# Optimization experiments

Hardware: AMD Instinct MI355X
Metric: run time of the kernel (lower is better)

The kernel has to match this reference:

```python
import jax, jax.numpy as jnp
import numpy as np

H = 768  # hidden size
L = 2    # num layers


def _lstm_layer(xs, ms, Wih, Whh, bih, bhh):
    """xs: [S,B,in], ms: [S,B,H] mask. Returns (outputs [S,B,H], (hT, cT)).
    PyTorch LSTMCell gate order: i, f, g, o. Zero initial state (module default),
    so the reset term init_hidden*(1-mask) is identically zero."""
    B = xs.shape[1]
    h0 = jnp.zeros((B, H), xs.dtype)
    c0 = jnp.zeros((B, H), xs.dtype)
    # Precompute input projections for all timesteps in one big GEMM.
    x_proj = jnp.einsum('sbi,gi->sbg', xs, Wih) + bih + bhh  # [S,B,4H]

    def step(carry, inp):
        h, c = carry
        xp, mt = inp
        gates = xp + h @ Whh.T  # [B,4H]
        i, f, g, o = jnp.split(gates, 4, axis=-1)
        i = jax.nn.sigmoid(i)
        f = jax.nn.sigmoid(f)
        g = jnp.tanh(g)
        o = jax.nn.sigmoid(o)
        c_next = (f * c + i * g)
        h_next = o * jnp.tanh(c_next)
        # mask-based state reset (h0=c0=0 -> pure multiply)
        h_next = h_next * mt
        c_next = c_next * mt
        return (h_next, c_next), h_next

    (hT, cT), outs = jax.lax.scan(step, (h0, c0), (x_proj, ms))
    return outs, (hT, cT)


def setup_inputs() -> dict:
    key = jax.random.key(0)
    ks = jax.random.split(key, 5)
    s = 0.05
    return {
        'x': jax.random.normal(ks[0], (64, 512, 768), jnp.float32),
        'mask': jnp.ones((64, 512), jnp.float32),
        'W_ih': jax.random.normal(ks[1], (L, 4 * H, 768), jnp.float32) * s,
        'W_hh': jax.random.normal(ks[2], (L, 4 * H, H), jnp.float32) * s,
        'b_ih': jax.random.normal(ks[3], (L, 4 * H), jnp.float32) * s,
        'b_hh': jax.random.normal(ks[4], (L, 4 * H), jnp.float32) * s,
    }


def reference(x, mask, W_ih, W_hh, b_ih, b_hh):
    # batch_first=True: transpose to [S,B,...]
    xs = jnp.transpose(x, (1, 0, 2))          # [S,B,in]
    ms = jnp.transpose(mask, (1, 0))[:, :, None]  # [S,B,1]
    ms = jnp.broadcast_to(ms, ms.shape[:2] + (H,))  # [S,B,H]
    hn, cn = [], []
    inp = xs
    for l in range(L):
        outs, (hT, cT) = _lstm_layer(inp, ms, W_ih[l], W_hh[l], b_ih[l], b_hh[l])
        hn.append(hT)
        cn.append(cT)
        inp = outs
    output = jnp.transpose(inp, (1, 0, 2))  # [B,S,H]
    return output, (jnp.stack(hn, 0), jnp.stack(cn, 0))
```

## Files before the change

### kernel.cpp

```cpp
#include <hip/hip_runtime.h>
#include <hip/hip_bf16.h>


#define HID 768
#define FH  3072
#define SEQ 512
#define BAT 64
#define GB  16
#define WPG 64
#define CPW 12
#define NWG 256
#define TPB 768
#define WBLK (12*64*8)

typedef __attribute__((ext_vector_type(8))) __bf16 bf16x8;
typedef __attribute__((ext_vector_type(4))) float f32x4;
typedef unsigned int u32;
typedef unsigned long long u64;

__device__ __forceinline__ float sigm(float z) { return 1.f / (1.f + __expf(-z)); }
__device__ __forceinline__ float tanh_fast(float x) {
  float a = fabsf(x);
  float e = __expf(-2.f * a);
  float t = (1.f - e) / (1.f + e);
  return copysignf(t, x);
}
__device__ __forceinline__ unsigned short bfbits(__bf16 b) {
  union { __bf16 b; unsigned short s; } u; u.b = b; return u.s;
}
__device__ __forceinline__ __bf16 bits2bf(unsigned short s) {
  union { unsigned short s; __bf16 b; } u; u.s = s; return u.b;
}
__device__ __forceinline__ u32 packsplit(float v) {
  __bf16 h = (__bf16)v;
  __bf16 l = (__bf16)(v - (float)h);
  return ((u32)bfbits(h) << 16) | (u32)bfbits(l);
}
__device__ __forceinline__ void split8(const float* p, bf16x8& hi, bf16x8& lo) {
  const float4* q = (const float4*)p;
  float4 a = q[0], b = q[1];
  float v[8] = {a.x, a.y, a.z, a.w, b.x, b.y, b.z, b.w};
#pragma unroll
  for (int i = 0; i < 8; ++i) {
    __bf16 h = (__bf16)v[i];
    hi[i] = h;
    lo[i] = (__bf16)(v[i] - (float)h);
  }
}
__device__ __forceinline__ void unpack8(const u32 w[8], bf16x8& hi, bf16x8& lo) {
#pragma unroll
  for (int i = 0; i < 8; ++i) {
    hi[i] = bits2bf((unsigned short)(w[i] >> 16));
    lo[i] = bits2bf((unsigned short)(w[i] & 0xffffu));
  }
}
__device__ __forceinline__ bf16x8 q2b(uint4 q) {
  union { uint4 q; bf16x8 v; } u; u.q = q; return u.v;
}
__device__ __forceinline__ uint4 b2q(bf16x8 v) {
  union { bf16x8 v; uint4 q; } u; u.v = v; return u.q;
}

__global__ void pack_wh(const float* __restrict__ Whh, u32* __restrict__ wpk) {
  const int NT = 2*64*6*12*64;
  int t = blockIdx.x * blockDim.x + threadIdx.x;
  if (t >= NT) return;
  int lane = t & 63; int r = t >> 6;
  int kk = r % 12;  r /= 12;
  int lane6 = r % 6; r /= 6;
  int wid = r % 64; r /= 64;
  int layer = r;
  int tile = lane6 >> 1, half = lane6 & 1;
  int l15 = lane & 15, lhi = lane >> 4;
  int colA = wid*CPW + tile*4 + (l15 >> 2);
  int qA   = l15 & 3;
  int row  = qA*HID + colA;
  int k    = half*384 + kk*32 + lhi*8;
  const float* W = Whh + (size_t)layer*FH*HID;
  bf16x8 hi, lo;
  split8(W + (size_t)row*HID + k, hi, lo);
  u32* dst = wpk + (size_t)t * 8;
  *(uint4*)dst       = b2q(hi);
  *(uint4*)(dst + 4) = b2q(lo);
}

template<int FMT>
__device__ __forceinline__ f32x4 proj384(const float* xf, const u32* xp,
                                         size_t base,
                                         const bf16x8* ah, const bf16x8* al) {
  f32x4 acc[4];
#pragma unroll
  for (int r = 0; r < 4; ++r) acc[r] = f32x4{0.f, 0.f, 0.f, 0.f};
#pragma unroll
  for (int kk = 0; kk < 12; ++kk) {
    bf16x8 bhi, blo;
    if constexpr (FMT == 0) {
      split8(xf + base + kk*32, bhi, blo);
    } else {
      const uint4* p = (const uint4*)(xp + base + kk*32);
      uint4 A = p[0], B = p[1];
      u32 w[8] = {A.x, A.y, A.z, A.w, B.x, B.y, B.z, B.w};
      unpack8(w, bhi, blo);
    }
    acc[(3*kk+0)&3] = __builtin_amdgcn_mfma_f32_16x16x32_bf16(ah[kk], bhi, acc[(3*kk+0)&3], 0, 0, 0);
    acc[(3*kk+1)&3] = __builtin_amdgcn_mfma_f32_16x16x32_bf16(al[kk], bhi, acc[(3*kk+1)&3], 0, 0, 0);
    acc[(3*kk+2)&3] = __builtin_amdgcn_mfma_f32_16x16x32_bf16(ah[kk], blo, acc[(3*kk+2)&3], 0, 0, 0);
  }
  return acc[0] + acc[1] + acc[2] + acc[3];
}

template<int XFMT, int WRITE_OUT, int RING>
__attribute__((amdgpu_waves_per_eu(3, 3)))
__global__ void __launch_bounds__(TPB)
lstm_scan(const float* __restrict__ xf,
          const u32* __restrict__ xp,
          const float* __restrict__ mask,
          const float* __restrict__ Wih,
          const u32* __restrict__ whpk,
          const float* __restrict__ bih,
          const float* __restrict__ bhh,
          u32* __restrict__ hdst,
          const u32* __restrict__ hsrc,
          float* __restrict__ out_f,
          float* __restrict__ hn,
          float* __restrict__ cn,
          int* __restrict__ flags)
{
  __shared__ f32x4 xacc_l[24][3][64];
  __shared__ f32x4 xpart_l[3][64];
  __shared__ f32x4 hpart_l[2][3][64];

  const int wg  = blockIdx.x;
  const int grp = wg >> 6;
  const int wid = wg & 63;
  const int tid = threadIdx.x;
  const int wv  = tid >> 6;
  const int l   = tid & 63;
  const int l15 = l & 15;
  const int lhi = l >> 4;

  const bool isx  = (wv < 6);
  const int lane6 = isx ? wv : (wv - 6);
  const int tile  = lane6 >> 1;
  const int half  = lane6 & 1;
  const int kofs  = half * 384;

  const int colA = wid*CPW + tile*4 + (l15 >> 2);
  const int qA   = l15 & 3;
  bf16x8 ah[12], al[12];
  if (isx) {
    const float* wrow = Wih + (size_t)(qA*HID + colA)*HID + kofs + lhi*8;
#pragma unroll
    for (int kk = 0; kk < 12; ++kk) split8(wrow + kk*32, ah[kk], al[kk]);
  }
  const u32* wbh = whpk + ((size_t)wid*6 + lane6) * WBLK;

  const int batch = grp*GB + l15;
  const int colO  = wid*CPW + tile*4 + lhi;
  float bias4[4] = {0.f, 0.f, 0.f, 0.f};
  if (!isx && half == 1) {
#pragma unroll
    for (int j = 0; j < 4; ++j) bias4[j] = bih[j*HID + colO] + bhh[j*HID + colO];
  }
  const float* mrow = mask + batch*SEQ;
  int* gflags = flags + grp*WPG;

  const int kb = kofs + lhi*8;

  float cstate = 0.f;

  {
    f32x4 px{0.f, 0.f, 0.f, 0.f};
    if (isx) {
      size_t base = (XFMT == 0) ? ((size_t)batch*SEQ)*HID + kb
                                : ((size_t)batch)*HID + kb;
      px = proj384<XFMT>(xf, xp, base, ah, al);
      if (half == 0) xpart_l[tile][l] = px;
    }
    __syncthreads();
    if (isx && half == 1) xacc_l[0][tile][l] = px + xpart_l[tile][l];
    __syncthreads();
  }

#pragma unroll 1
  for (int s = 0; s < SEQ; ++s) {
    f32x4 xa{0.f, 0.f, 0.f, 0.f};
    if (isx && s + 1 < SEQ) {
      size_t base = (XFMT == 0) ? ((size_t)batch*SEQ + (s+1))*HID + kb
                                : ((size_t)(s+1)*BAT + batch)*HID + kb;
      xa = proj384<XFMT>(xf, xp, base, ah, al);
      if (half == 0) xpart_l[tile][l] = xa;
    }
    if (!isx && lane6 == 0 && s > 0) {
      while (true) {
        int v = __hip_atomic_load(gflags + l, __ATOMIC_RELAXED, __HIP_MEMORY_SCOPE_AGENT);
        if (__all(v >= s)) break;
        __builtin_amdgcn_s_sleep(1);
      }
    }
    __syncthreads();

    f32x4 ha{0.f, 0.f, 0.f, 0.f};
    if (!isx && s > 0) {
      size_t base = RING ? ((size_t)((s-1) & 1)*BAT + batch)*HID + kb
                         : ((size_t)(s-1)*BAT + batch)*HID + kb;
      f32x4 acc[4];
#pragma unroll
      for (int r = 0; r < 4; ++r) acc[r] = f32x4{0.f, 0.f, 0.f, 0.f};
#pragma unroll
      for (int kk = 0; kk < 12; ++kk) {
        const uint4* wp = (const uint4*)(wbh + (size_t)(kk*64 + l)*8);
        bf16x8 Ah = q2b(wp[0]);
        bf16x8 Al = q2b(wp[1]);
        u32 w[8];
        if constexpr (RING) {
          const u64* sp = (const u64*)(hsrc + base + kk*32);
          u64 a = __hip_atomic_load(sp,     __ATOMIC_RELAXED, __HIP_MEMORY_SCOPE_AGENT);
          u64 b = __hip_atomic_load(sp + 1, __ATOMIC_RELAXED, __HIP_MEMORY_SCOPE_AGENT);
          u64 c = __hip_atomic_load(sp + 2, __ATOMIC_RELAXED, __HIP_MEMORY_SCOPE_AGENT);
          u64 d = __hip_atomic_load(sp + 3, __ATOMIC_RELAXED, __HIP_MEMORY_SCOPE_AGENT);
          w[0]=(u32)a; w[1]=(u32)(a>>32); w[2]=(u32)b; w[3]=(u32)(b>>32);
          w[4]=(u32)c; w[5]=(u32)(c>>32); w[6]=(u32)d; w[7]=(u32)(d>>32);
        } else {
          const uint4* p = (const uint4*)(hsrc + base + kk*32);
          uint4 A = p[0], B = p[1];
          w[0]=A.x; w[1]=A.y; w[2]=A.z; w[3]=A.w;
          w[4]=B.x; w[5]=B.y; w[6]=B.z; w[7]=B.w;
        }
        bf16x8 bhi, blo;
        unpack8(w, bhi, blo);
        acc[(3*kk+0)&3] = __builtin_amdgcn_mfma_f32_16x16x32_bf16(Ah, bhi, acc[(3*kk+0)&3], 0, 0, 0);
        acc[(3*kk+1)&3] = __builtin_amdgcn_mfma_f32_16x16x32_bf16(Al, bhi, acc[(3*kk+1)&3], 0, 0, 0);
        acc[(3*kk+2)&3] = __builtin_amdgcn_mfma_f32_16x16x32_bf16(Ah, blo, acc[(3*kk+2)&3], 0, 0, 0);
      }
      ha = acc[0] + acc[1] + acc[2] + acc[3];
      if (half == 0) hpart_l[s & 1][tile][l] = ha;
    }
    if (isx && half == 1 && s + 1 < SEQ)
      xacc_l[(s+1) & 3][tile][l] = xa + xpart_l[tile][l];
    __syncthreads();

    if (!isx && half == 1) {
      f32x4 z = xacc_l[s & 3][tile][l];
      if (s > 0) z = z + ha + hpart_l[s & 1][tile][l];
      float zi = z[0] + bias4[0], zf = z[1] + bias4[1];
      float zg = z[2] + bias4[2], zo = z[3] + bias4[3];
      float iv = sigm(zi), fv = sigm(zf), gv = tanh_fast(zg), ov = sigm(zo);
      float c  = fv*cstate + iv*gv;
      float hv = ov * tanh_fast(c);
      float m  = mrow[s];
      hv *= m; c *= m; cstate = c;

      u32 hw = packsplit(hv);
      size_t wrow = RING ? ((size_t)(s & 1)*BAT + batch)*HID + colO
                         : ((size_t)s*BAT + batch)*HID + colO;
      __hip_atomic_store(hdst + wrow, hw,
                         __ATOMIC_RELAXED, __HIP_MEMORY_SCOPE_AGENT);
      if constexpr (WRITE_OUT) {
        __builtin_nontemporal_store(hv, out_f + ((size_t)batch*SEQ + s)*HID + colO);
      }
      if (s == SEQ - 1) {
        hn[batch*HID + colO] = hv;
        cn[batch*HID + colO] = c;
      }
      asm volatile("s_waitcnt vmcnt(0)" ::: "memory");
    }
    __syncthreads();
    if (tid == 0)
      __hip_atomic_store(gflags + wid, s + 1,
                         __ATOMIC_RELAXED, __HIP_MEMORY_SCOPE_AGENT);
  }
}

extern "C" void kernel_launch(void* const* d_in, const int* in_sizes, int n_in,
                              void* d_out, int out_size, void* d_ws, size_t ws_size,
                              hipStream_t stream) {
  const float* x    = (const float*)d_in[0];
  const float* mask = (const float*)d_in[1];
  const float* Wih  = (const float*)d_in[2];
  const float* Whh  = (const float*)d_in[3];
  const float* bih  = (const float*)d_in[4];
  const float* bhh  = (const float*)d_in[5];
  float* out = (float*)d_out;

  char* ws = (char*)d_ws;
  const size_t WPKH_B  = (size_t)2*64*6*WBLK*4;
  const size_t STREAM_B = (size_t)SEQ*BAT*HID*4;
  const size_t RING_B  = (size_t)2*BAT*HID*4;

  u32* wpk = (u32*)ws;
  u32* opk = (u32*)(ws + WPKH_B);
  const bool big = ws_size >= WPKH_B + 2*STREAM_B + RING_B + 65536;
  u32* h1  = (u32*)(ws + WPKH_B + STREAM_B);
  int* flags = big ? (int*)(ws + WPKH_B + 2*STREAM_B)
                   : (int*)(ws + WPKH_B + STREAM_B + RING_B);

  (void)hipMemsetAsync(flags, 0, 2*NWG*sizeof(int), stream);
  pack_wh<<<2304, 256, 0, stream>>>(Whh, wpk);

  float* hn = out + 25165824;
  float* cn = out + 25165824 + 98304;

  const size_t WLH = (size_t)64*6*WBLK;

  lstm_scan<0, 0, 0><<<dim3(NWG), dim3(TPB), 0, stream>>>(
      x, nullptr, mask, Wih, wpk, bih, bhh,
      opk, opk, nullptr, hn, cn, flags);

  if (big) {
    lstm_scan<1, 1, 0><<<dim3(NWG), dim3(TPB), 0, stream>>>(
        nullptr, opk, mask, Wih + (size_t)FH*HID, wpk + WLH, bih + FH, bhh + FH,
        h1, h1, out, hn + 49152, cn + 49152, flags + NWG);
  } else {
    lstm_scan<1, 1, 1><<<dim3(NWG), dim3(TPB), 0, stream>>>(
        nullptr, opk, mask, Wih + (size_t)FH*HID, wpk + WLH, bih + FH, bhh + FH,
        h1, h1, out, hn + 49152, cn + 49152, flags + NWG);
  }
}
```

Baseline: 13.67 ms.

## Split recurrent GEMM across twelve K-slice waves and pack input weights

Raises the workgroup to 16 waves. Twelve waves each compute a 64-wide K-slice of the recurrent h·Whh product for all three column tiles, three waves compute the input projection for the next step, and one wave polls the cross-workgroup flags. Input-projection weights are now pre-packed into split bf16 hi/lo form by the packing kernel and streamed from global memory rather than held in registers. The aim is to shorten the serial per-step critical path by spreading the recurrent MFMA chain over more waves. In exchange the gate waves must reduce twelve LDS partials, the input weights are re-read every step, occupancy is pinned at four waves per EU, and a dummy LDS pad array is added to inflate shared memory.

```diff
diff --git a/kernel.cpp b/kernel.cpp
--- a/kernel.cpp
+++ b/kernel.cpp
@@ -8,10 +8,8 @@
 #define BAT 64
 #define GB  16
 #define WPG 64
-#define CPW 12
 #define NWG 256
-#define TPB 768
-#define WBLK (12*64*8)
+#define TPB 1024
 
 typedef __attribute__((ext_vector_type(8))) __bf16 bf16x8;
 typedef __attribute__((ext_vector_type(4))) float f32x4;
@@ -61,74 +59,65 @@
   union { bf16x8 v; uint4 q; } u; u.v = v; return u.q;
 }
 
-__global__ void pack_wh(const float* __restrict__ Whh, u32* __restrict__ wpk) {
-  const int NT = 2*64*6*12*64;
-  int t = blockIdx.x * blockDim.x + threadIdx.x;
-  if (t >= NT) return;
-  int lane = t & 63; int r = t >> 6;
-  int kk = r % 12;  r /= 12;
-  int lane6 = r % 6; r /= 6;
-  int wid = r % 64; r /= 64;
-  int layer = r;
-  int tile = lane6 >> 1, half = lane6 & 1;
+__global__ void pack_w(const float* __restrict__ Wih,
+                       const float* __restrict__ Whh,
+                       u32* __restrict__ wpk) {
+  int g = blockIdx.x * blockDim.x + threadIdx.x;
+  const int NT = 2 * 9216 * 64;
+  if (g >= NT) return;
+  int lane = g & 63;
+  int sl = g >> 6;
+  int region = sl / 9216;
+  int sr = sl % 9216;
   int l15 = lane & 15, lhi = lane >> 4;
-  int colA = wid*CPW + tile*4 + (l15 >> 2);
-  int qA   = l15 & 3;
-  int row  = qA*HID + colA;
-  int k    = half*384 + kk*32 + lhi*8;
-  const float* W = Whh + (size_t)layer*FH*HID;
+  int k, t, wid, layer;
+  const float* W;
+  if (region == 0) {
+    int c  = sr % 8;
+    t      = (sr / 8) % 3;
+    int xw = (sr / 24) % 3;
+    wid    = (sr / 72) % 64;
+    layer  = sr / 4608;
+    k = xw*256 + c*32 + lhi*8;
+    W = Wih + (size_t)layer*FH*HID;
+  } else {
+    int c  = sr % 2;
+    t      = (sr / 2) % 3;
+    int j  = (sr / 6) % 12;
+    wid    = (sr / 72) % 64;
+    layer  = sr / 4608;
+    k = j*64 + c*32 + lhi*8;
+    W = Whh + (size_t)layer*FH*HID;
+  }
+  int row = (l15 & 3)*HID + wid*12 + t*4 + (l15 >> 2);
   bf16x8 hi, lo;
   split8(W + (size_t)row*HID + k, hi, lo);
-  u32* dst = wpk + (size_t)t * 8;
+  u32* dst = wpk + ((size_t)region*9216 + sr)*512 + lane*8;
   *(uint4*)dst       = b2q(hi);
   *(uint4*)(dst + 4) = b2q(lo);
 }
 
-template<int FMT>
-__device__ __forceinline__ f32x4 proj384(const float* xf, const u32* xp,
-                                         size_t base,
-                                         const bf16x8* ah, const bf16x8* al) {
-  f32x4 acc[4];
-#pragma unroll
-  for (int r = 0; r < 4; ++r) acc[r] = f32x4{0.f, 0.f, 0.f, 0.f};
-#pragma unroll
-  for (int kk = 0; kk < 12; ++kk) {
-    bf16x8 bhi, blo;
-    if constexpr (FMT == 0) {
-      split8(xf + base + kk*32, bhi, blo);
-    } else {
-      const uint4* p = (const uint4*)(xp + base + kk*32);
-      uint4 A = p[0], B = p[1];
-      u32 w[8] = {A.x, A.y, A.z, A.w, B.x, B.y, B.z, B.w};
-      unpack8(w, bhi, blo);
-    }
-    acc[(3*kk+0)&3] = __builtin_amdgcn_mfma_f32_16x16x32_bf16(ah[kk], bhi, acc[(3*kk+0)&3], 0, 0, 0);
-    acc[(3*kk+1)&3] = __builtin_amdgcn_mfma_f32_16x16x32_bf16(al[kk], bhi, acc[(3*kk+1)&3], 0, 0, 0);
-    acc[(3*kk+2)&3] = __builtin_amdgcn_mfma_f32_16x16x32_bf16(ah[kk], blo, acc[(3*kk+2)&3], 0, 0, 0);
-  }
-  return acc[0] + acc[1] + acc[2] + acc[3];
-}
+#define MFMA16 __builtin_amdgcn_mfma_f32_16x16x32_bf16
 
 template<int XFMT, int WRITE_OUT, int RING>
-__attribute__((amdgpu_waves_per_eu(3, 3)))
+__attribute__((amdgpu_waves_per_eu(4, 4)))
 __global__ void __launch_bounds__(TPB)
 lstm_scan(const float* __restrict__ xf,
           const u32* __restrict__ xp,
           const float* __restrict__ mask,
-          const float* __restrict__ Wih,
+          const u32* __restrict__ wipk,
           const u32* __restrict__ whpk,
           const float* __restrict__ bih,
           const float* __restrict__ bhh,
           u32* __restrict__ hdst,
           const u32* __restrict__ hsrc,
           float* __restrict__ out_f,
-          float* __restrict__ hn,
-          float* __restrict__ cn,
+          float* __restrict__ hn, float* __restrict__ cn,
           int* __restrict__ flags)
 {
-  __shared__ f32x4 xacc_l[24][3][64];
-  __shared__ f32x4 xpart_l[3][64];
-  __shared__ f32x4 hpart_l[2][3][64];
+  __shared__ f32x4 xring[4][3][3][64];
+  __shared__ f32x4 hpart[12][3][64];
+  __shared__ f32x4 padlds[512];
 
   const int wg  = blockIdx.x;
   const int grp = wg >> 6;
@@ -139,59 +128,68 @@
   const int l15 = l & 15;
   const int lhi = l >> 4;
 
-  const bool isx  = (wv < 6);
-  const int lane6 = isx ? wv : (wv - 6);
-  const int tile  = lane6 >> 1;
-  const int half  = lane6 & 1;
-  const int kofs  = half * 384;
-
-  const int colA = wid*CPW + tile*4 + (l15 >> 2);
-  const int qA   = l15 & 3;
-  bf16x8 ah[12], al[12];
-  if (isx) {
-    const float* wrow = Wih + (size_t)(qA*HID + colA)*HID + kofs + lhi*8;
-#pragma unroll
-    for (int kk = 0; kk < 12; ++kk) split8(wrow + kk*32, ah[kk], al[kk]);
-  }
-  const u32* wbh = whpk + ((size_t)wid*6 + lane6) * WBLK;
+  if ((int)blockIdx.x == -1) padlds[tid & 511] = hpart[0][0][0];
+
+  const bool ish  = (wv < 12);
+  const bool isxw = (wv >= 12 && wv < 15);
+  const int j  = wv;
+  const int xw = wv - 12;
 
   const int batch = grp*GB + l15;
-  const int colO  = wid*CPW + tile*4 + lhi;
+  const u32* wbj = whpk + (size_t)(wid*12 + (ish  ? j  : 0))*6*512;
+  const u32* wbx = wipk + (size_t)(wid*3  + (isxw ? xw : 0))*24*512;
+
+  const int colO = wid*12 + (isxw ? xw : 0)*4 + lhi;
   float bias4[4] = {0.f, 0.f, 0.f, 0.f};
-  if (!isx && half == 1) {
-#pragma unroll
-    for (int j = 0; j < 4; ++j) bias4[j] = bih[j*HID + colO] + bhh[j*HID + colO];
+  if (isxw) {
+#pragma unroll
+    for (int r = 0; r < 4; ++r) bias4[r] = bih[r*HID + colO] + bhh[r*HID + colO];
   }
   const float* mrow = mask + batch*SEQ;
   int* gflags = flags + grp*WPG;
-
-  const int kb = kofs + lhi*8;
-
   float cstate = 0.f;
 
-  {
-    f32x4 px{0.f, 0.f, 0.f, 0.f};
-    if (isx) {
-      size_t base = (XFMT == 0) ? ((size_t)batch*SEQ)*HID + kb
-                                : ((size_t)batch)*HID + kb;
-      px = proj384<XFMT>(xf, xp, base, ah, al);
-      if (half == 0) xpart_l[tile][l] = px;
+  auto xproj = [&](int sstep, int slot) {
+    f32x4 a0{0.f,0.f,0.f,0.f}, a1{0.f,0.f,0.f,0.f}, a2{0.f,0.f,0.f,0.f};
+#pragma unroll
+    for (int c = 0; c < 8; ++c) {
+      bf16x8 bhi, blo;
+      if constexpr (XFMT == 0) {
+        const float* src = xf + ((size_t)batch*SEQ + sstep)*HID + xw*256 + c*32 + lhi*8;
+        split8(src, bhi, blo);
+      } else {
+        const u32* src = xp + ((size_t)sstep*BAT + batch)*HID + xw*256 + c*32 + lhi*8;
+        uint4 A = *(const uint4*)src, B = *(const uint4*)(src + 4);
+        u32 w[8] = {A.x,A.y,A.z,A.w,B.x,B.y,B.z,B.w};
+        unpack8(w, bhi, blo);
+      }
+      {
+        const uint4* wp = (const uint4*)(wbx + (size_t)(0*8 + c)*512 + l*8);
+        bf16x8 Ah = q2b(wp[0]), Al = q2b(wp[1]);
+        a0 = MFMA16(Ah, bhi, a0, 0,0,0); a0 = MFMA16(Al, bhi, a0, 0,0,0); a0 = MFMA16(Ah, blo, a0, 0,0,0);
+      }
+      {
+        const uint4* wp = (const uint4*)(wbx + (size_t)(1*8 + c)*512 + l*8);
+        bf16x8 Ah = q2b(wp[0]), Al = q2b(wp[1]);
+        a1 = MFMA16(Ah, bhi, a1, 0,0,0); a1 = MFMA16(Al, bhi, a1, 0,0,0); a1 = MFMA16(Ah, blo, a1, 0,0,0);
+      }
+      {
+        const uint4* wp = (const uint4*)(wbx + (size_t)(2*8 + c)*512 + l*8);
+        bf16x8 Ah = q2b(wp[0]), Al = q2b(wp[1]);
+        a2 = MFMA16(Ah, bhi, a2, 0,0,0); a2 = MFMA16(Al, bhi, a2, 0,0,0); a2 = MFMA16(Ah, blo, a2, 0,0,0);
+      }
     }
-    __syncthreads();
-    if (isx && half == 1) xacc_l[0][tile][l] = px + xpart_l[tile][l];
-    __syncthreads();
-  }
+    xring[slot][xw][0][l] = a0;
+    xring[slot][xw][1][l] = a1;
+    xring[slot][xw][2][l] = a2;
+  };
+
+  if (isxw) xproj(0, 0);
+  __syncthreads();
 
 #pragma unroll 1
   for (int s = 0; s < SEQ; ++s) {
-    f32x4 xa{0.f, 0.f, 0.f, 0.f};
-    if (isx && s + 1 < SEQ) {
-      size_t base = (XFMT == 0) ? ((size_t)batch*SEQ + (s+1))*HID + kb
-                                : ((size_t)(s+1)*BAT + batch)*HID + kb;
-      xa = proj384<XFMT>(xf, xp, base, ah, al);
-      if (half == 0) xpart_l[tile][l] = xa;
-    }
-    if (!isx && lane6 == 0 && s > 0) {
+    if (wv == 15 && s > 0) {
       while (true) {
         int v = __hip_atomic_load(gflags + l, __ATOMIC_RELAXED, __HIP_MEMORY_SCOPE_AGENT);
         if (__all(v >= s)) break;
@@ -200,49 +198,56 @@
     }
     __syncthreads();
 
-    f32x4 ha{0.f, 0.f, 0.f, 0.f};
-    if (!isx && s > 0) {
-      size_t base = RING ? ((size_t)((s-1) & 1)*BAT + batch)*HID + kb
-                         : ((size_t)(s-1)*BAT + batch)*HID + kb;
-      f32x4 acc[4];
-#pragma unroll
-      for (int r = 0; r < 4; ++r) acc[r] = f32x4{0.f, 0.f, 0.f, 0.f};
-#pragma unroll
-      for (int kk = 0; kk < 12; ++kk) {
-        const uint4* wp = (const uint4*)(wbh + (size_t)(kk*64 + l)*8);
-        bf16x8 Ah = q2b(wp[0]);
-        bf16x8 Al = q2b(wp[1]);
+    if (ish && s > 0) {
+      f32x4 a0{0.f,0.f,0.f,0.f}, a1{0.f,0.f,0.f,0.f}, a2{0.f,0.f,0.f,0.f};
+#pragma unroll
+      for (int c = 0; c < 2; ++c) {
         u32 w[8];
         if constexpr (RING) {
-          const u64* sp = (const u64*)(hsrc + base + kk*32);
-          u64 a = __hip_atomic_load(sp,     __ATOMIC_RELAXED, __HIP_MEMORY_SCOPE_AGENT);
-          u64 b = __hip_atomic_load(sp + 1, __ATOMIC_RELAXED, __HIP_MEMORY_SCOPE_AGENT);
-          u64 c = __hip_atomic_load(sp + 2, __ATOMIC_RELAXED, __HIP_MEMORY_SCOPE_AGENT);
-          u64 d = __hip_atomic_load(sp + 3, __ATOMIC_RELAXED, __HIP_MEMORY_SCOPE_AGENT);
-          w[0]=(u32)a; w[1]=(u32)(a>>32); w[2]=(u32)b; w[3]=(u32)(b>>32);
-          w[4]=(u32)c; w[5]=(u32)(c>>32); w[6]=(u32)d; w[7]=(u32)(d>>32);
+          const u64* sp = (const u64*)(hsrc + ((size_t)((s-1)&1)*BAT + batch)*HID + j*64 + c*32 + lhi*8);
+          u64 qa = __hip_atomic_load(sp,   __ATOMIC_RELAXED, __HIP_MEMORY_SCOPE_AGENT);
+          u64 qb = __hip_atomic_load(sp+1, __ATOMIC_RELAXED, __HIP_MEMORY_SCOPE_AGENT);
+          u64 qc = __hip_atomic_load(sp+2, __ATOMIC_RELAXED, __HIP_MEMORY_SCOPE_AGENT);
+          u64 qd = __hip_atomic_load(sp+3, __ATOMIC_RELAXED, __HIP_MEMORY_SCOPE_AGENT);
+          w[0]=(u32)qa; w[1]=(u32)(qa>>32); w[2]=(u32)qb; w[3]=(u32)(qb>>32);
+          w[4]=(u32)qc; w[5]=(u32)(qc>>32); w[6]=(u32)qd; w[7]=(u32)(qd>>32);
         } else {
-          const uint4* p = (const uint4*)(hsrc + base + kk*32);
-          uint4 A = p[0], B = p[1];
+          const u32* sp = hsrc + ((size_t)(s-1)*BAT + batch)*HID + j*64 + c*32 + lhi*8;
+          uint4 A = *(const uint4*)sp, B = *(const uint4*)(sp + 4);
           w[0]=A.x; w[1]=A.y; w[2]=A.z; w[3]=A.w;
           w[4]=B.x; w[5]=B.y; w[6]=B.z; w[7]=B.w;
         }
         bf16x8 bhi, blo;
         unpack8(w, bhi, blo);
-        acc[(3*kk+0)&3] = __builtin_amdgcn_mfma_f32_16x16x32_bf16(Ah, bhi, acc[(3*kk+0)&3], 0, 0, 0);
-        acc[(3*kk+1)&3] = __builtin_amdgcn_mfma_f32_16x16x32_bf16(Al, bhi, acc[(3*kk+1)&3], 0, 0, 0);
-        acc[(3*kk+2)&3] = __builtin_amdgcn_mfma_f32_16x16x32_bf16(Ah, blo, acc[(3*kk+2)&3], 0, 0, 0);
-      }
-      ha = acc[0] + acc[1] + acc[2] + acc[3];
-      if (half == 0) hpart_l[s & 1][tile][l] = ha;
+        {
+          const uint4* wp = (const uint4*)(wbj + (size_t)(0*2 + c)*512 + l*8);
+          bf16x8 Ah = q2b(wp[0]), Al = q2b(wp[1]);
+          a0 = MFMA16(Ah, bhi, a0, 0,0,0); a0 = MFMA16(Al, bhi, a0, 0,0,0); a0 = MFMA16(Ah, blo, a0, 0,0,0);
+        }
+        {
+          const uint4* wp = (const uint4*)(wbj + (size_t)(1*2 + c)*512 + l*8);
+          bf16x8 Ah = q2b(wp[0]), Al = q2b(wp[1]);
+          a1 = MFMA16(Ah, bhi, a1, 0,0,0); a1 = MFMA16(Al, bhi, a1, 0,0,0); a1 = MFMA16(Ah, blo, a1, 0,0,0);
+        }
+        {
+          const uint4* wp = (const uint4*)(wbj + (size_t)(2*2 + c)*512 + l*8);
+          bf16x8 Ah = q2b(wp[0]), Al = q2b(wp[1]);
+          a2 = MFMA16(Ah, bhi, a2, 0,0,0); a2 = MFMA16(Al, bhi, a2, 0,0,0); a2 = MFMA16(Ah, blo, a2, 0,0,0);
+        }
+      }
+      hpart[j][0][l] = a0;
+      hpart[j][1][l] = a1;
+      hpart[j][2][l] = a2;
     }
-    if (isx && half == 1 && s + 1 < SEQ)
-      xacc_l[(s+1) & 3][tile][l] = xa + xpart_l[tile][l];
+    if (isxw && s + 1 < SEQ) xproj(s + 1, (s + 1) & 3);
     __syncthreads();
 
-    if (!isx && half == 1) {
-      f32x4 z = xacc_l[s & 3][tile][l];
-      if (s > 0) z = z + ha + hpart_l[s & 1][tile][l];
+    if (isxw) {
+      f32x4 z = xring[s & 3][0][xw][l] + xring[s & 3][1][xw][l] + xring[s & 3][2][xw][l];
+      if (s > 0) {
+#pragma unroll
+        for (int jj = 0; jj < 12; ++jj) z = z + hpart[jj][xw][l];
+      }
       float zi = z[0] + bias4[0], zf = z[1] + bias4[1];
       float zg = z[2] + bias4[2], zo = z[3] + bias4[3];
       float iv = sigm(zi), fv = sigm(zf), gv = tanh_fast(zg), ov = sigm(zo);
@@ -284,36 +289,39 @@
   float* out = (float*)d_out;
 
   char* ws = (char*)d_ws;
-  const size_t WPKH_B  = (size_t)2*64*6*WBLK*4;
+  const size_t WPK_B   = (size_t)2*9216*512*4;
   const size_t STREAM_B = (size_t)SEQ*BAT*HID*4;
   const size_t RING_B  = (size_t)2*BAT*HID*4;
 
   u32* wpk = (u32*)ws;
-  u32* opk = (u32*)(ws + WPKH_B);
-  const bool big = ws_size >= WPKH_B + 2*STREAM_B + RING_B + 65536;
-  u32* h1  = (u32*)(ws + WPKH_B + STREAM_B);
-  int* flags = big ? (int*)(ws + WPKH_B + 2*STREAM_B)
-                   : (int*)(ws + WPKH_B + STREAM_B + RING_B);
+  u32* opk = (u32*)(ws + WPK_B);
+  const bool big = ws_size >= WPK_B + 2*STREAM_B + 4096;
+  u32* h1  = (u32*)(ws + WPK_B + STREAM_B);
+  int* flags = big ? (int*)(ws + WPK_B + 2*STREAM_B)
+                   : (int*)(ws + WPK_B + STREAM_B + RING_B);
 
   (void)hipMemsetAsync(flags, 0, 2*NWG*sizeof(int), stream);
-  pack_wh<<<2304, 256, 0, stream>>>(Whh, wpk);
+  pack_w<<<4608, 256, 0, stream>>>(Wih, Whh, wpk);
 
   float* hn = out + 25165824;
   float* cn = out + 25165824 + 98304;
 
-  const size_t WLH = (size_t)64*6*WBLK;
+  const u32* wipk0 = wpk;
+  const u32* wipk1 = wpk + (size_t)4608*512;
+  const u32* whpk0 = wpk + (size_t)9216*512;
+  const u32* whpk1 = wpk + (size_t)13824*512;
 
   lstm_scan<0, 0, 0><<<dim3(NWG), dim3(TPB), 0, stream>>>(
-      x, nullptr, mask, Wih, wpk, bih, bhh,
+      x, nullptr, mask, wipk0, whpk0, bih, bhh,
       opk, opk, nullptr, hn, cn, flags);
 
   if (big) {
     lstm_scan<1, 1, 0><<<dim3(NWG), dim3(TPB), 0, stream>>>(
-        nullptr, opk, mask, Wih + (size_t)FH*HID, wpk + WLH, bih + FH, bhh + FH,
+        nullptr, opk, mask, wipk1, whpk1, bih + FH, bhh + FH,
         h1, h1, out, hn + 49152, cn + 49152, flags + NWG);
   } else {
     lstm_scan<1, 1, 1><<<dim3(NWG), dim3(TPB), 0, stream>>>(
-        nullptr, opk, mask, Wih + (size_t)FH*HID, wpk + WLH, bih + FH, bhh + FH,
+        nullptr, opk, mask, wipk1, whpk1, bih + FH, bhh + FH,
         h1, h1, out, hn + 49152, cn + 49152, flags + NWG);
   }
 }
```

Measured after the change: 13.76 ms. No clear change (+0.6%).
